# Optimization experiments

Measured on AMD Instinct MI355X. Metric: run time of the kernel, lower is better.

Reference implementation:

```python
import jax, jax.numpy as jnp
import numpy as np

N = 500000
V = 50000
GF = 64
OC = 256

def _lin(key, din, dout):
    k1, k2 = jax.random.split(key)
    w = jax.random.normal(k1, (din, dout), dtype=jnp.float32) * 0.02
    b = jax.random.normal(k2, (dout,), dtype=jnp.float32) * 0.02
    return w, b

def setup_inputs() -> dict:
    key = jax.random.key(0)
    ks = jax.random.split(key, 12)
    inp_feat = jax.random.normal(ks[0], (N, 6), dtype=jnp.float32)
    vox2point_idx = jax.random.randint(ks[1], (N,), 0, V, dtype=jnp.int32)
    w1x, b1x = _lin(ks[2], 3, GF)
    w2x, b2x = _lin(ks[3], GF, OC // 8)
    w1r, b1r = _lin(ks[4], 3, GF)
    w2r, b2r = _lin(ks[5], GF, OC // 8)
    wax, bax = _lin(ks[6], OC // 4, OC // 8)
    war, bar = _lin(ks[7], OC // 4, OC // 8)
    wv1, bv1 = _lin(ks[8], OC // 2, OC // 2)
    w3, b3 = _lin(ks[9], OC, OC)
    w4, b4 = _lin(ks[10], OC, OC)
    wv2, bv2 = _lin(ks[11], OC, OC)
    return dict(inp_feat=inp_feat, vox2point_idx=vox2point_idx, num_vox=V,
                w1x=w1x, b1x=b1x, w2x=w2x, b2x=b2x,
                w1r=w1r, b1r=b1r, w2r=w2r, b2r=b2r,
                wax=wax, bax=bax, war=war, bar=bar,
                wv1=wv1, bv1=bv1, w3=w3, b3=b3, w4=w4, b4=b4,
                wv2=wv2, bv2=bv2)

def reference(inp_feat, vox2point_idx, num_vox,
              w1x, b1x, w2x, b2x, w1r, b1r, w2r, b2r,
              wax, bax, war, bar, wv1, bv1, w3, b3, w4, b4, wv2, bv2):
    relu = jax.nn.relu
    xyz = inp_feat[:, :3]
    rgb = inp_feat[:, 3:]
    fx = relu(relu(xyz @ w1x + b1x) @ w2x + b2x)   # [N, 32]
    fr = relu(relu(rgb @ w1r + b1r) @ w2r + b2r)   # [N, 32]
    comb = jnp.concatenate([fx, fr], axis=-1)       # [N, 64]
    pf2 = jnp.concatenate([
        fx, fx * jax.nn.sigmoid(comb @ wax + bax),
        fr, fr * jax.nn.sigmoid(comb @ war + bar)], axis=-1)  # [N, 128]
    # scatter-max to voxels; torch_scatter fills empty segments with 0 and
    # pf2 >= 0 elementwise, so clamp -inf (jax empty fill) to 0 for parity.
    vox = jax.ops.segment_max(pf2, vox2point_idx, num_segments=num_vox)
    vox = jnp.maximum(vox, 0.0)                     # [V, 128]
    vox = relu(vox @ wv1 + bv1)
    pg = vox[vox2point_idx]                          # gather back [N, 128]
    pf3 = jnp.concatenate([pg, pf2], axis=-1)        # [N, 256]
    pf5 = relu(relu(pf3 @ w3 + b3) @ w4 + b4)        # [N, 256]
    vox2 = jax.ops.segment_max(pf5, vox2point_idx, num_segments=num_vox)
    vox2 = jnp.maximum(vox2, 0.0)
    return relu(vox2 @ wv2 + bv2)                    # [V, 256]
```

## Files before the change

### kernel.cpp

```cpp
#include <hip/hip_runtime.h>

#define NPTS 500000
#define NVOX 50000
#define NBLK 196

typedef unsigned short u16;
typedef unsigned int u32;
typedef __attribute__((ext_vector_type(8))) short short8;
typedef __attribute__((ext_vector_type(4))) float floatx4;
typedef __attribute__((ext_vector_type(4))) unsigned int uintx4;
typedef __attribute__((ext_vector_type(2))) unsigned int uintx2;

__device__ __forceinline__ u16 f2bf(float f) {
    u32 u = __float_as_uint(f);
    u = u + 0x7fffu + ((u >> 16) & 1u);
    return (u16)(u >> 16);
}

#if defined(__has_builtin)
#if __has_builtin(__builtin_amdgcn_cvt_pk_bf16_f32)
#define HAVE_PKBF 1
#endif
#endif

__device__ __forceinline__ u32 pkbf(float a, float b) {
#ifdef HAVE_PKBF
    typedef __attribute__((ext_vector_type(2))) __bf16 bf16x2;
    bf16x2 v = __builtin_amdgcn_cvt_pk_bf16_f32(a, b);
    u32 r; __builtin_memcpy(&r, &v, 4);
    return r;
#else
    return (u32)f2bf(a) | ((u32)f2bf(b) << 16);
#endif
}

__device__ __forceinline__ void wswz(const float* __restrict__ W, u16* __restrict__ Wf, int N, int t) {
    int k = t / N, n = t - k * N;
    int kk = k >> 5, q = (k >> 3) & 3, j = k & 7;
    Wf[((size_t)((kk * 4 + q) * N + n) << 3) + j] = f2bf(W[t]);
}

__global__ __launch_bounds__(256) void k_wprep(
    const float* __restrict__ w3, const float* __restrict__ w4,
    const float* __restrict__ wv1, const float* __restrict__ wv2,
    const float* __restrict__ w2x, const float* __restrict__ w2r,
    const float* __restrict__ wax, const float* __restrict__ war,
    u16* __restrict__ w3f, u16* __restrict__ w4f, u16* __restrict__ wv1f, u16* __restrict__ wv2f,
    u16* __restrict__ wcatf, u16* __restrict__ wattf)
{
    int t = blockIdx.x * 256 + threadIdx.x;
    if (t < 65536) { wswz(w3, w3f, 256, t); return; }  t -= 65536;
    if (t < 65536) { wswz(w4, w4f, 256, t); return; }  t -= 65536;
    if (t < 65536) { wswz(wv2, wv2f, 256, t); return; } t -= 65536;
    if (t < 16384) { wswz(wv1, wv1f, 128, t); return; } t -= 16384;
    if (t < 8192) {
        int k = t >> 6, n = t & 63;
        float v;
        if (k < 64) v = (n < 32) ? w2x[k * 32 + n] : 0.f;
        else        v = (n >= 32) ? w2r[(k - 64) * 32 + (n - 32)] : 0.f;
        int kk = k >> 5, q = (k >> 3) & 3, j = k & 7;
        wcatf[((size_t)((kk * 4 + q) * 64 + n) << 3) + j] = f2bf(v);
        return;
    }
    t -= 8192;
    if (t < 4096) {
        int k = t >> 6, n = t & 63;
        float v = (n < 32) ? wax[k * 32 + n] : war[k * 32 + (n - 32)];
        int kk = k >> 5, q = (k >> 3) & 3, j = k & 7;
        wattf[((size_t)((kk * 4 + q) * 64 + n) << 3) + j] = f2bf(v);
    }
}

__global__ void k_hist(const int* __restrict__ idx, int* __restrict__ hcnt) {
    int i = blockIdx.x * 256 + threadIdx.x;
    if (i < NPTS) atomicAdd(&hcnt[idx[i]], 1);
}

__global__ __launch_bounds__(256) void k_scan1(const int* __restrict__ hcnt, int* __restrict__ bsum) {
    __shared__ int wsum[4];
    int t = threadIdx.x;
    int i = blockIdx.x * 256 + t;
    int c = (i < NVOX) ? hcnt[i] : 0;
    #pragma unroll
    for (int d = 32; d >= 1; d >>= 1) c += __shfl_xor(c, d, 64);
    if ((t & 63) == 0) wsum[t >> 6] = c;
    __syncthreads();
    if (t == 0) bsum[blockIdx.x] = wsum[0] + wsum[1] + wsum[2] + wsum[3];
}

__global__ __launch_bounds__(256) void k_scan2(const int* __restrict__ bsum, int* __restrict__ boff) {
    __shared__ int wsum[4];
    int t = threadIdx.x, lane = t & 63, w = t >> 6;
    int c = (t < NBLK) ? bsum[t] : 0;
    int v = c;
    #pragma unroll
    for (int d = 1; d < 64; d <<= 1) {
        int o = __shfl_up(v, d, 64);
        if (lane >= d) v += o;
    }
    if (lane == 63) wsum[w] = v;
    __syncthreads();
    int wo = 0;
    #pragma unroll
    for (int k = 0; k < 4; k++) if (k < w) wo += wsum[k];
    if (t < NBLK) boff[t] = wo + v - c;
}

__global__ __launch_bounds__(256) void k_scan3(const int* __restrict__ hcnt, const int* __restrict__ boff,
                                               int* __restrict__ cur) {
    __shared__ int wsum[4];
    int t = threadIdx.x, lane = t & 63, w = t >> 6;
    int i = blockIdx.x * 256 + t;
    int c = (i < NVOX) ? hcnt[i] : 0;
    int v = c;
    #pragma unroll
    for (int d = 1; d < 64; d <<= 1) {
        int o = __shfl_up(v, d, 64);
        if (lane >= d) v += o;
    }
    if (lane == 63) wsum[w] = v;
    __syncthreads();
    int wo = 0;
    #pragma unroll
    for (int k = 0; k < 4; k++) if (k < w) wo += wsum[k];
    if (i < NVOX) cur[i] = boff[blockIdx.x] + wo + v - c;
}

__global__ void k_scatter(const int* __restrict__ idx, int* __restrict__ cur,
                          int* __restrict__ sptid, int* __restrict__ svid) {
    int i = blockIdx.x * 256 + threadIdx.x;
    if (i < NPTS) {
        int v = idx[i];
        int pos = atomicAdd(&cur[v], 1);
        sptid[pos] = i;
        svid[pos] = v;
    }
}

__global__ __launch_bounds__(512) void k_pointfeat(
    const float* __restrict__ inp, const int* __restrict__ sptid, const int* __restrict__ svid,
    const float* __restrict__ w1x, const float* __restrict__ b1x,
    const float* __restrict__ w1r, const float* __restrict__ b1r,
    const u16* __restrict__ wcatf, const float* __restrict__ b2x, const float* __restrict__ b2r,
    const u16* __restrict__ wattf, const float* __restrict__ bax, const float* __restrict__ bar,
    u16* __restrict__ pf2s, float* __restrict__ voxmax)
{
    __shared__ u16 hbuf[128 * 136];
    __shared__ float wl[512];
    __shared__ int lvid[128];
    int t = threadIdx.x;
    int i0 = blockIdx.x * 128;
    int mcnt = NPTS - i0; if (mcnt > 128) mcnt = 128;
    {
        float v;
        if (t < 192)      v = w1x[t];
        else if (t < 256) v = b1x[t - 192];
        else if (t < 448) v = w1r[t - 256];
        else              v = b1r[t - 448];
        wl[t] = v;
    }
    if (t < 128) lvid[t] = (t < mcnt) ? svid[i0 + t] : -1;
    __syncthreads();
    {
        int m = t >> 2, c = t & 3;
        float x0 = 0, x1 = 0, x2 = 0, r0 = 0, r1 = 0, r2 = 0;
        if (m < mcnt) {
            const float* p = inp + (size_t)sptid[i0 + m] * 6;
            x0 = p[0]; x1 = p[1]; x2 = p[2]; r0 = p[3]; r1 = p[4]; r2 = p[5];
        }
        u16* hb = &hbuf[m * 136 + c * 16];
        #pragma unroll
        for (int jp = 0; jp < 8; jp++) {
            int c0 = c * 16 + 2 * jp, c1 = c0 + 1;
            float hx0 = fmaxf(wl[192 + c0] + x0 * wl[c0] + x1 * wl[64 + c0] + x2 * wl[128 + c0], 0.f);
            float hx1 = fmaxf(wl[192 + c1] + x0 * wl[c1] + x1 * wl[64 + c1] + x2 * wl[128 + c1], 0.f);
            float hr0 = fmaxf(wl[448 + c0] + r0 * wl[256 + c0] + r1 * wl[320 + c0] + r2 * wl[384 + c0], 0.f);
            float hr1 = fmaxf(wl[448 + c1] + r0 * wl[256 + c1] + r1 * wl[320 + c1] + r2 * wl[384 + c1], 0.f);
            *(u32*)(hb + 2 * jp)      = pkbf(hx0, hx1);
            *(u32*)(hb + 64 + 2 * jp) = pkbf(hr0, hr1);
        }
    }
    __syncthreads();
    int wave = t >> 6, l = t & 63, q = l >> 4, lm = l & 15;
    int n = (wave & 3) * 16 + lm;
    int rh = (wave >> 2) * 64;
    floatx4 acc[4];
    #pragma unroll
    for (int a = 0; a < 4; a++) acc[a] = (floatx4){0.f, 0.f, 0.f, 0.f};
    #pragma unroll
    for (int kk = 0; kk < 4; kk++) {
        short8 bfrag = *(const short8*)&wcatf[(size_t)((kk * 4 + q) * 64 + n) << 3];
        #pragma unroll
        for (int tm = 0; tm < 4; tm++) {
            short8 afrag = *(const short8*)&hbuf[(rh + tm * 16 + lm) * 136 + kk * 32 + q * 8];
            acc[tm] = __builtin_amdgcn_mfma_f32_16x16x32_bf16(afrag, bfrag, acc[tm], 0, 0, 0);
        }
    }
    float bv = (n < 32) ? b2x[n] : b2r[n - 32];
    float comb_keep[4][4];
    #pragma unroll
    for (int tm = 0; tm < 4; tm++)
        #pragma unroll
        for (int r = 0; r < 4; r++)
            comb_keep[tm][r] = fmaxf(acc[tm][r] + bv, 0.f);
    __syncthreads();
    #pragma unroll
    for (int tm = 0; tm < 4; tm++)
        #pragma unroll
        for (int r = 0; r < 4; r++) {
            int m = rh + tm * 16 + q * 4 + r;
            hbuf[m * 136 + n] = f2bf(comb_keep[tm][r]);
        }
    __syncthreads();
    floatx4 acc2[4];
    #pragma unroll
    for (int a = 0; a < 4; a++) acc2[a] = (floatx4){0.f, 0.f, 0.f, 0.f};
    #pragma unroll
    for (int kk = 0; kk < 2; kk++) {
        short8 bfrag = *(const short8*)&wattf[(size_t)((kk * 4 + q) * 64 + n) << 3];
        #pragma unroll
        for (int tm = 0; tm < 4; tm++) {
            short8 afrag = *(const short8*)&hbuf[(rh + tm * 16 + lm) * 136 + kk * 32 + q * 8];
            acc2[tm] = __builtin_amdgcn_mfma_f32_16x16x32_bf16(afrag, bfrag, acc2[tm], 0, 0, 0);
        }
    }
    __syncthreads();
    float bv2 = (n < 32) ? bax[n] : bar[n - 32];
    int pp = (n < 32) ? n : 32 + n;
    #pragma unroll
    for (int tm = 0; tm < 4; tm++)
        #pragma unroll
        for (int r = 0; r < 4; r++) {
            float att = acc2[tm][r] + bv2;
            float sg = 1.f / (1.f + __expf(-att));
            float plain = comb_keep[tm][r];
            float gated = plain * sg;
            int m = rh + tm * 16 + q * 4 + r;
            hbuf[m * 136 + pp] = f2bf(plain);
            hbuf[m * 136 + pp + 32] = f2bf(gated);
        }
    __syncthreads();
    {
        int row = t >> 2, seg = t & 3;
        if (row < mcnt) {
            const u16* src = &hbuf[row * 136 + seg * 32];
            u16* dst = pf2s + (size_t)(i0 + row) * 128 + seg * 32;
            *(uintx4*)dst = *(const uintx4*)src;
            *(uintx4*)(dst + 8) = *(const uintx4*)(src + 8);
        }
    }
    {
        int c2 = t & 63;
        int h = t >> 6;
        int r0 = h * 16;
        int r1 = r0 + 16; if (r1 > mcnt) r1 = mcnt;
        u32 mlo = 0, mhi = 0;
        int pvid = -1;
        for (int r = r0; r < r1; r++) {
            int vid = lvid[r];
            if (vid != pvid) {
                if (pvid >= 0) {
                    int* addr = (int*)(voxmax + (size_t)pvid * 128 + 2 * c2);
                    if (mlo) atomicMax(addr, (int)(mlo << 16));
                    if (mhi) atomicMax(addr + 1, (int)(mhi << 16));
                }
                pvid = vid; mlo = 0; mhi = 0;
            }
            u32 u = *(const u32*)&hbuf[r * 136 + 2 * c2];
            u32 lo = u & 0xffffu, hi = u >> 16;
            mlo = lo > mlo ? lo : mlo;
            mhi = hi > mhi ? hi : mhi;
        }
        if (pvid >= 0) {
            int* addr = (int*)(voxmax + (size_t)pvid * 128 + 2 * c2);
            if (mlo) atomicMax(addr, (int)(mlo << 16));
            if (mhi) atomicMax(addr + 1, (int)(mhi << 16));
        }
    }
}

template<int K, int N, bool ABF16, bool OUT_BF16>
__global__ __launch_bounds__(256) void k_gemm_relu(
    const void* __restrict__ Ap, const u16* __restrict__ Wf,
    const float* __restrict__ bias, void* __restrict__ outp, int M)
{
    constexpr int STRIDE = K + 8;
    constexpr int TN = N / 64;
    constexpr int KSTEPS = K / 32;
    constexpr int CW = K / 4;
    __shared__ u16 lds[64 * STRIDE];
    int i0 = blockIdx.x * 64;
    int mcnt = M - i0; if (mcnt > 64) mcnt = 64;
    int t = threadIdx.x;
    {
        int row = t >> 2, cseg = t & 3;
        u16* dst = &lds[row * STRIDE + cseg * CW];
        if (row < mcnt) {
            if (ABF16) {
                const u16* src = (const u16*)Ap + (size_t)(i0 + row) * K + cseg * CW;
                #pragma unroll
                for (int c = 0; c < CW / 8; c++)
                    *(uintx4*)(dst + c * 8) = *(const uintx4*)(src + c * 8);
            } else {
                const float* src = (const float*)Ap + (size_t)(i0 + row) * K + cseg * CW;
                #pragma unroll
                for (int c = 0; c < CW / 8; c++) {
                    float4 v0 = *(const float4*)(src + c * 8);
                    float4 v1 = *(const float4*)(src + c * 8 + 4);
                    uintx4 rr = {pkbf(v0.x, v0.y), pkbf(v0.z, v0.w), pkbf(v1.x, v1.y), pkbf(v1.z, v1.w)};
                    *(uintx4*)(dst + c * 8) = rr;
                }
            }
        } else {
            uintx4 z = {0, 0, 0, 0};
            #pragma unroll
            for (int c = 0; c < CW / 8; c++) *(uintx4*)(dst + c * 8) = z;
        }
    }
    __syncthreads();
    int wave = t >> 6, l = t & 63;
    int q = l >> 4, lm = l & 15;
    int wn0 = wave * (N / 4);
    floatx4 acc[4][TN];
    #pragma unroll
    for (int a = 0; a < 4; a++)
        #pragma unroll
        for (int b = 0; b < TN; b++) acc[a][b] = (floatx4){0.f, 0.f, 0.f, 0.f};
    #pragma unroll
    for (int kk = 0; kk < KSTEPS; kk++) {
        short8 afrag[4], bfrag[TN];
        #pragma unroll
        for (int tm = 0; tm < 4; tm++)
            afrag[tm] = *(const short8*)&lds[(tm * 16 + lm) * STRIDE + kk * 32 + q * 8];
        #pragma unroll
        for (int tn = 0; tn < TN; tn++)
            bfrag[tn] = *(const short8*)&Wf[(size_t)((kk * 4 + q) * N + wn0 + tn * 16 + lm) * 8];
        #pragma unroll
        for (int tm = 0; tm < 4; tm++)
            #pragma unroll
            for (int tn = 0; tn < TN; tn++)
                acc[tm][tn] = __builtin_amdgcn_mfma_f32_16x16x32_bf16(afrag[tm], bfrag[tn], acc[tm][tn], 0, 0, 0);
    }
    #pragma unroll
    for (int tm = 0; tm < 4; tm++)
        #pragma unroll
        for (int tn = 0; tn < TN; tn++) {
            int n = wn0 + tn * 16 + lm;
            float bv = bias[n];
            #pragma unroll
            for (int r = 0; r < 4; r++) {
                int m = tm * 16 + q * 4 + r;
                if (m < mcnt) {
                    float v = fmaxf(acc[tm][tn][r] + bv, 0.f);
                    if (OUT_BF16) ((u16*)outp)[(size_t)(i0 + m) * N + n] = f2bf(v);
                    else          ((float*)outp)[(size_t)(i0 + m) * N + n] = v;
                }
            }
        }
}

__global__ __launch_bounds__(512) void k_pointmlp(
    const u16* __restrict__ voxf, const u16* __restrict__ pf2s, const int* __restrict__ svid,
    const u16* __restrict__ w3f, const float* __restrict__ b3,
    const u16* __restrict__ w4f, const float* __restrict__ b4,
    float* __restrict__ vox2)
{
    constexpr int STRIDE = 264;
    __shared__ u16 lds[64 * STRIDE];
    __shared__ int lvid[64];
    __shared__ float bl[512];
    int i0 = blockIdx.x * 64;
    int mcnt = NPTS - i0; if (mcnt > 64) mcnt = 64;
    int t = threadIdx.x;
    if (t < 64) lvid[t] = (t < mcnt) ? svid[i0 + t] : -1;
    bl[t] = (t < 256) ? b3[t] : b4[t - 256];
    {
        int row = t >> 3, cseg = t & 7;
        u16* dst = &lds[row * STRIDE + cseg * 32];
        if (row < mcnt) {
            const u16* src;
            if (cseg < 4) src = voxf + (size_t)svid[i0 + row] * 128 + cseg * 32;
            else          src = pf2s + (size_t)(i0 + row) * 128 + (cseg - 4) * 32;
            #pragma unroll
            for (int c = 0; c < 4; c++)
                *(uintx4*)(dst + c * 8) = *(const uintx4*)(src + c * 8);
        } else {
            uintx4 z = {0, 0, 0, 0};
            #pragma unroll
            for (int c = 0; c < 4; c++) *(uintx4*)(dst + c * 8) = z;
        }
    }
    __syncthreads();
    int wave = t >> 6, l = t & 63;
    int q = l >> 4, lm = l & 15;
    int wm0 = wave * 32;
    floatx4 acc[2][4];
    #pragma unroll
    for (int a = 0; a < 2; a++)
        #pragma unroll
        for (int b = 0; b < 4; b++) acc[a][b] = (floatx4){0.f, 0.f, 0.f, 0.f};
    #pragma unroll
    for (int kk = 0; kk < 8; kk++) {
        short8 wfrag[2], bfrag[4];
        #pragma unroll
        for (int tm = 0; tm < 2; tm++)
            wfrag[tm] = *(const short8*)&w3f[(size_t)((kk * 4 + q) * 256 + wm0 + tm * 16 + lm) * 8];
        #pragma unroll
        for (int tn = 0; tn < 4; tn++)
            bfrag[tn] = *(const short8*)&lds[(tn * 16 + lm) * STRIDE + kk * 32 + q * 8];
        #pragma unroll
        for (int tm = 0; tm < 2; tm++)
            #pragma unroll
            for (int tn = 0; tn < 4; tn++)
                acc[tm][tn] = __builtin_amdgcn_mfma_f32_16x16x32_bf16(wfrag[tm], bfrag[tn], acc[tm][tn], 0, 0, 0);
    }
    __syncthreads();
    #pragma unroll
    for (int tm = 0; tm < 2; tm++) {
        float4 bq = *(const float4*)&bl[wm0 + tm * 16 + 4 * q];
        #pragma unroll
        for (int tn = 0; tn < 4; tn++) {
            u32 lo = pkbf(fmaxf(acc[tm][tn][0] + bq.x, 0.f), fmaxf(acc[tm][tn][1] + bq.y, 0.f));
            u32 hi = pkbf(fmaxf(acc[tm][tn][2] + bq.z, 0.f), fmaxf(acc[tm][tn][3] + bq.w, 0.f));
            *(uintx2*)&lds[(tn * 16 + lm) * STRIDE + wm0 + tm * 16 + 4 * q] = (uintx2){lo, hi};
        }
    }
    __syncthreads();
    floatx4 acc2[2][4];
    #pragma unroll
    for (int a = 0; a < 2; a++)
        #pragma unroll
        for (int b = 0; b < 4; b++) acc2[a][b] = (floatx4){0.f, 0.f, 0.f, 0.f};
    #pragma unroll
    for (int kk = 0; kk < 8; kk++) {
        short8 wfrag[2], bfrag[4];
        #pragma unroll
        for (int tm = 0; tm < 2; tm++)
            wfrag[tm] = *(const short8*)&w4f[(size_t)((kk * 4 + q) * 256 + wm0 + tm * 16 + lm) * 8];
        #pragma unroll
        for (int tn = 0; tn < 4; tn++)
            bfrag[tn] = *(const short8*)&lds[(tn * 16 + lm) * STRIDE + kk * 32 + q * 8];
        #pragma unroll
        for (int tm = 0; tm < 2; tm++)
            #pragma unroll
            for (int tn = 0; tn < 4; tn++)
                acc2[tm][tn] = __builtin_amdgcn_mfma_f32_16x16x32_bf16(wfrag[tm], bfrag[tn], acc2[tm][tn], 0, 0, 0);
    }
    __syncthreads();
    #pragma unroll
    for (int tm = 0; tm < 2; tm++) {
        float4 bq = *(const float4*)&bl[256 + wm0 + tm * 16 + 4 * q];
        #pragma unroll
        for (int tn = 0; tn < 4; tn++) {
            u32 lo = pkbf(fmaxf(acc2[tm][tn][0] + bq.x, 0.f), fmaxf(acc2[tm][tn][1] + bq.y, 0.f));
            u32 hi = pkbf(fmaxf(acc2[tm][tn][2] + bq.z, 0.f), fmaxf(acc2[tm][tn][3] + bq.w, 0.f));
            *(uintx2*)&lds[(tn * 16 + lm) * STRIDE + wm0 + tm * 16 + 4 * q] = (uintx2){lo, hi};
        }
    }
    __syncthreads();
    {
        int c2 = t & 127;
        int h = t >> 7;
        int r0 = h * 16;
        int r1 = r0 + 16; if (r1 > mcnt) r1 = mcnt;
        u32 mlo = 0, mhi = 0;
        int pvid = -1;
        for (int r = r0; r < r1; r++) {
            int vid = lvid[r];
            if (vid != pvid) {
                if (pvid >= 0) {
                    int* addr = (int*)(vox2 + (size_t)pvid * 256 + 2 * c2);
                    if (mlo) atomicMax(addr, (int)(mlo << 16));
                    if (mhi) atomicMax(addr + 1, (int)(mhi << 16));
                }
                pvid = vid; mlo = 0; mhi = 0;
            }
            u32 u = *(const u32*)&lds[r * STRIDE + 2 * c2];
            u32 lo = u & 0xffffu, hi = u >> 16;
            mlo = lo > mlo ? lo : mlo;
            mhi = hi > mhi ? hi : mhi;
        }
        if (pvid >= 0) {
            int* addr = (int*)(vox2 + (size_t)pvid * 256 + 2 * c2);
            if (mlo) atomicMax(addr, (int)(mlo << 16));
            if (mhi) atomicMax(addr + 1, (int)(mhi << 16));
        }
    }
}

extern "C" void kernel_launch(void* const* d_in, const int* in_sizes, int n_in,
                              void* d_out, int out_size, void* d_ws, size_t ws_size,
                              hipStream_t stream) {
    const float* inp = (const float*)d_in[0];
    const int*   idx = (const int*)d_in[1];
    const float* w1x = (const float*)d_in[3];  const float* b1x = (const float*)d_in[4];
    const float* w2x = (const float*)d_in[5];  const float* b2x = (const float*)d_in[6];
    const float* w1r = (const float*)d_in[7];  const float* b1r = (const float*)d_in[8];
    const float* w2r = (const float*)d_in[9];  const float* b2r = (const float*)d_in[10];
    const float* wax = (const float*)d_in[11]; const float* bax = (const float*)d_in[12];
    const float* war = (const float*)d_in[13]; const float* bar = (const float*)d_in[14];
    const float* wv1 = (const float*)d_in[15]; const float* bv1 = (const float*)d_in[16];
    const float* w3  = (const float*)d_in[17]; const float* b3  = (const float*)d_in[18];
    const float* w4  = (const float*)d_in[19]; const float* b4  = (const float*)d_in[20];
    const float* wv2 = (const float*)d_in[21]; const float* bv2 = (const float*)d_in[22];
    float* out = (float*)d_out;

    char* ws = (char*)d_ws;
    u16*   pf2s   = (u16*)ws;   ws += (size_t)NPTS * 128 * sizeof(u16);
    float* voxmax = (float*)ws; ws += (size_t)NVOX * 128 * sizeof(float);
    u16*   voxf   = (u16*)ws;   ws += (size_t)NVOX * 128 * sizeof(u16);
    float* vox2   = (float*)ws; ws += (size_t)NVOX * 256 * sizeof(float);
    u16*   w3f    = (u16*)ws;   ws += 65536 * sizeof(u16);
    u16*   w4f    = (u16*)ws;   ws += 65536 * sizeof(u16);
    u16*   wv1f   = (u16*)ws;   ws += 16384 * sizeof(u16);
    u16*   wv2f   = (u16*)ws;   ws += 65536 * sizeof(u16);
    u16*   wcatf  = (u16*)ws;   ws += 8192 * sizeof(u16);
    u16*   wattf  = (u16*)ws;   ws += 4096 * sizeof(u16);
    int*   hcnt   = (int*)ws;   ws += (size_t)NVOX * sizeof(int);
    int*   cur    = (int*)ws;   ws += (size_t)NVOX * sizeof(int);
    int*   bsum   = (int*)ws;   ws += (size_t)NBLK * sizeof(int);
    int*   boff   = (int*)ws;   ws += (size_t)NBLK * sizeof(int);
    int*   sptid  = (int*)ws;   ws += (size_t)NPTS * sizeof(int);
    int*   svid   = (int*)ws;   ws += (size_t)NPTS * sizeof(int);

    hipMemsetAsync(hcnt, 0, (size_t)NVOX * sizeof(int), stream);
    hipMemsetAsync(voxmax, 0, (size_t)NVOX * 128 * sizeof(float), stream);
    hipMemsetAsync(vox2, 0, (size_t)NVOX * 256 * sizeof(float), stream);

    k_wprep<<<880, 256, 0, stream>>>(w3, w4, wv1, wv2, w2x, w2r, wax, war,
                                     w3f, w4f, wv1f, wv2f, wcatf, wattf);

    k_hist<<<(NPTS + 255) / 256, 256, 0, stream>>>(idx, hcnt);
    k_scan1<<<NBLK, 256, 0, stream>>>(hcnt, bsum);
    k_scan2<<<1, 256, 0, stream>>>(bsum, boff);
    k_scan3<<<NBLK, 256, 0, stream>>>(hcnt, boff, cur);
    k_scatter<<<(NPTS + 255) / 256, 256, 0, stream>>>(idx, cur, sptid, svid);

    k_pointfeat<<<(NPTS + 127) / 128, 512, 0, stream>>>(
        inp, sptid, svid, w1x, b1x, w1r, b1r, wcatf, b2x, b2r, wattf, bax, bar, pf2s, voxmax);

    k_gemm_relu<128, 128, false, true><<<(NVOX + 63) / 64, 256, 0, stream>>>(
        (const void*)voxmax, wv1f, bv1, (void*)voxf, NVOX);

    k_pointmlp<<<(NPTS + 63) / 64, 512, 0, stream>>>(
        voxf, pf2s, svid, w3f, b3, w4f, b4, vox2);

    k_gemm_relu<256, 256, false, false><<<(NVOX + 63) / 64, 256, 0, stream>>>(
        (const void*)vox2, wv2f, bv2, (void*)out, NVOX);
}
```

Measured before the change: 514.9 us.

## Switch point MLP to 32x32x16 MFMA with 256-thread blocks and XOR-swizzled LDS

The fused point-MLP kernel now uses 32x32x16 bf16 MFMA tiles instead of 16x16x32, with 4 waves per 64-point block. Each wave covers 32 points by 128 channels. The w3/w4 weight swizzle is changed to match the new K-fragment layout, and LDS rows use an XOR chunk swizzle to cut bank conflicts on fragment reads and writes. Fewer, larger MFMAs reuse each B fragment across four weight tiles. The cost is more accumulator registers per thread and half as many threads per block to issue loads and scatter-max atomics.

```diff
diff --git a/kernel.cpp b/kernel.cpp
--- a/kernel.cpp
+++ b/kernel.cpp
@@ -8,6 +8,7 @@
 typedef unsigned int u32;
 typedef __attribute__((ext_vector_type(8))) short short8;
 typedef __attribute__((ext_vector_type(4))) float floatx4;
+typedef __attribute__((ext_vector_type(16))) float floatx16;
 typedef __attribute__((ext_vector_type(4))) unsigned int uintx4;
 typedef __attribute__((ext_vector_type(2))) unsigned int uintx2;
 
@@ -40,6 +41,12 @@
     Wf[((size_t)((kk * 4 + q) * N + n) << 3) + j] = f2bf(W[t]);
 }
 
+__device__ __forceinline__ void wswz32(const float* __restrict__ W, u16* __restrict__ Wf, int N, int t) {
+    int k = t / N, n = t - k * N;
+    int kk = k >> 4, h = (k >> 3) & 1, j = k & 7;
+    Wf[((size_t)((kk * 2 + h) * N + n) << 3) + j] = f2bf(W[t]);
+}
+
 __global__ __launch_bounds__(256) void k_wprep(
     const float* __restrict__ w3, const float* __restrict__ w4,
     const float* __restrict__ wv1, const float* __restrict__ wv2,
@@ -49,8 +56,8 @@
     u16* __restrict__ wcatf, u16* __restrict__ wattf)
 {
     int t = blockIdx.x * 256 + threadIdx.x;
-    if (t < 65536) { wswz(w3, w3f, 256, t); return; }  t -= 65536;
-    if (t < 65536) { wswz(w4, w4f, 256, t); return; }  t -= 65536;
+    if (t < 65536) { wswz32(w3, w3f, 256, t); return; }  t -= 65536;
+    if (t < 65536) { wswz32(w4, w4f, 256, t); return; }  t -= 65536;
     if (t < 65536) { wswz(wv2, wv2f, 256, t); return; } t -= 65536;
     if (t < 16384) { wswz(wv1, wv1f, 128, t); return; } t -= 16384;
     if (t < 8192) {
@@ -359,7 +366,7 @@
         }
 }
 
-__global__ __launch_bounds__(512) void k_pointmlp(
+__global__ __launch_bounds__(256) void k_pointmlp(
     const u16* __restrict__ voxf, const u16* __restrict__ pf2s, const int* __restrict__ svid,
     const u16* __restrict__ w3f, const float* __restrict__ b3,
     const u16* __restrict__ w4f, const float* __restrict__ b4,
@@ -373,96 +380,101 @@
     int mcnt = NPTS - i0; if (mcnt > 64) mcnt = 64;
     int t = threadIdx.x;
     if (t < 64) lvid[t] = (t < mcnt) ? svid[i0 + t] : -1;
-    bl[t] = (t < 256) ? b3[t] : b4[t - 256];
-    {
-        int row = t >> 3, cseg = t & 7;
-        u16* dst = &lds[row * STRIDE + cseg * 32];
+    for (int s = t; s < 512; s += 256) bl[s] = (s < 256) ? b3[s] : b4[s - 256];
+    {
+        int row = t >> 2, cseg = t & 3;
+        int sig = (row >> 3) & 3;
         if (row < mcnt) {
             const u16* src;
-            if (cseg < 4) src = voxf + (size_t)svid[i0 + row] * 128 + cseg * 32;
-            else          src = pf2s + (size_t)(i0 + row) * 128 + (cseg - 4) * 32;
+            if (cseg < 2) src = voxf + (size_t)svid[i0 + row] * 128 + cseg * 64;
+            else          src = pf2s + (size_t)(i0 + row) * 128 + (cseg - 2) * 64;
             #pragma unroll
-            for (int c = 0; c < 4; c++)
-                *(uintx4*)(dst + c * 8) = *(const uintx4*)(src + c * 8);
+            for (int c = 0; c < 8; c++) {
+                int chunk = cseg * 8 + c;
+                *(uintx4*)&lds[row * STRIDE + (chunk ^ sig) * 8] = *(const uintx4*)(src + c * 8);
+            }
         } else {
             uintx4 z = {0, 0, 0, 0};
             #pragma unroll
-            for (int c = 0; c < 4; c++) *(uintx4*)(dst + c * 8) = z;
+            for (int c = 0; c < 8; c++) {
+                int chunk = cseg * 8 + c;
+                *(uintx4*)&lds[row * STRIDE + (chunk ^ sig) * 8] = z;
+            }
         }
     }
     __syncthreads();
     int wave = t >> 6, l = t & 63;
-    int q = l >> 4, lm = l & 15;
-    int wm0 = wave * 32;
-    floatx4 acc[2][4];
-    #pragma unroll
-    for (int a = 0; a < 2; a++)
-        #pragma unroll
-        for (int b = 0; b < 4; b++) acc[a][b] = (floatx4){0.f, 0.f, 0.f, 0.f};
-    #pragma unroll
-    for (int kk = 0; kk < 8; kk++) {
-        short8 wfrag[2], bfrag[4];
-        #pragma unroll
-        for (int tm = 0; tm < 2; tm++)
-            wfrag[tm] = *(const short8*)&w3f[(size_t)((kk * 4 + q) * 256 + wm0 + tm * 16 + lm) * 8];
-        #pragma unroll
-        for (int tn = 0; tn < 4; tn++)
-            bfrag[tn] = *(const short8*)&lds[(tn * 16 + lm) * STRIDE + kk * 32 + q * 8];
-        #pragma unroll
-        for (int tm = 0; tm < 2; tm++)
-            #pragma unroll
-            for (int tn = 0; tn < 4; tn++)
-                acc[tm][tn] = __builtin_amdgcn_mfma_f32_16x16x32_bf16(wfrag[tm], bfrag[tn], acc[tm][tn], 0, 0, 0);
-    }
-    __syncthreads();
-    #pragma unroll
-    for (int tm = 0; tm < 2; tm++) {
-        float4 bq = *(const float4*)&bl[wm0 + tm * 16 + 4 * q];
-        #pragma unroll
-        for (int tn = 0; tn < 4; tn++) {
-            u32 lo = pkbf(fmaxf(acc[tm][tn][0] + bq.x, 0.f), fmaxf(acc[tm][tn][1] + bq.y, 0.f));
-            u32 hi = pkbf(fmaxf(acc[tm][tn][2] + bq.z, 0.f), fmaxf(acc[tm][tn][3] + bq.w, 0.f));
-            *(uintx2*)&lds[(tn * 16 + lm) * STRIDE + wm0 + tm * 16 + 4 * q] = (uintx2){lo, hi};
-        }
-    }
-    __syncthreads();
-    floatx4 acc2[2][4];
-    #pragma unroll
-    for (int a = 0; a < 2; a++)
-        #pragma unroll
-        for (int b = 0; b < 4; b++) acc2[a][b] = (floatx4){0.f, 0.f, 0.f, 0.f};
-    #pragma unroll
-    for (int kk = 0; kk < 8; kk++) {
-        short8 wfrag[2], bfrag[4];
-        #pragma unroll
-        for (int tm = 0; tm < 2; tm++)
-            wfrag[tm] = *(const short8*)&w4f[(size_t)((kk * 4 + q) * 256 + wm0 + tm * 16 + lm) * 8];
-        #pragma unroll
-        for (int tn = 0; tn < 4; tn++)
-            bfrag[tn] = *(const short8*)&lds[(tn * 16 + lm) * STRIDE + kk * 32 + q * 8];
-        #pragma unroll
-        for (int tm = 0; tm < 2; tm++)
-            #pragma unroll
-            for (int tn = 0; tn < 4; tn++)
-                acc2[tm][tn] = __builtin_amdgcn_mfma_f32_16x16x32_bf16(wfrag[tm], bfrag[tn], acc2[tm][tn], 0, 0, 0);
-    }
-    __syncthreads();
-    #pragma unroll
-    for (int tm = 0; tm < 2; tm++) {
-        float4 bq = *(const float4*)&bl[256 + wm0 + tm * 16 + 4 * q];
-        #pragma unroll
-        for (int tn = 0; tn < 4; tn++) {
-            u32 lo = pkbf(fmaxf(acc2[tm][tn][0] + bq.x, 0.f), fmaxf(acc2[tm][tn][1] + bq.y, 0.f));
-            u32 hi = pkbf(fmaxf(acc2[tm][tn][2] + bq.z, 0.f), fmaxf(acc2[tm][tn][3] + bq.w, 0.f));
-            *(uintx2*)&lds[(tn * 16 + lm) * STRIDE + wm0 + tm * 16 + 4 * q] = (uintx2){lo, hi};
+    int am = l & 31, hh = l >> 5;
+    int cg = wave & 1;
+    int pg = wave >> 1;
+    int pbase = pg * 32;
+    int p = pbase + am;
+    int sigp = (p >> 3) & 3;
+    int chb = cg * 128;
+    floatx16 acc[4];
+    #pragma unroll
+    for (int a = 0; a < 4; a++)
+        #pragma unroll
+        for (int e = 0; e < 16; e++) acc[a][e] = 0.f;
+    #pragma unroll
+    for (int kk = 0; kk < 16; kk++) {
+        short8 bfrag = *(const short8*)&lds[p * STRIDE + (((kk * 2 + hh) ^ sigp) << 3)];
+        #pragma unroll
+        for (int tm = 0; tm < 4; tm++) {
+            short8 wfrag = *(const short8*)&w3f[(size_t)((kk * 2 + hh) * 256 + chb + tm * 32 + am) * 8];
+            acc[tm] = __builtin_amdgcn_mfma_f32_32x32x16_bf16(wfrag, bfrag, acc[tm], 0, 0, 0);
+        }
+    }
+    __syncthreads();
+    #pragma unroll
+    for (int tm = 0; tm < 4; tm++) {
+        int chb2 = chb + tm * 32;
+        #pragma unroll
+        for (int rg = 0; rg < 4; rg++) {
+            int ch0 = chb2 + 8 * rg + 4 * hh;
+            float4 bq = *(const float4*)&bl[ch0];
+            u32 lo = pkbf(fmaxf(acc[tm][4 * rg + 0] + bq.x, 0.f), fmaxf(acc[tm][4 * rg + 1] + bq.y, 0.f));
+            u32 hi = pkbf(fmaxf(acc[tm][4 * rg + 2] + bq.z, 0.f), fmaxf(acc[tm][4 * rg + 3] + bq.w, 0.f));
+            int chunk = (chb2 >> 3) + rg;
+            *(uintx2*)&lds[p * STRIDE + ((chunk ^ sigp) << 3) + 4 * hh] = (uintx2){lo, hi};
+        }
+    }
+    __syncthreads();
+    floatx16 acc2[4];
+    #pragma unroll
+    for (int a = 0; a < 4; a++)
+        #pragma unroll
+        for (int e = 0; e < 16; e++) acc2[a][e] = 0.f;
+    #pragma unroll
+    for (int kk = 0; kk < 16; kk++) {
+        short8 bfrag = *(const short8*)&lds[p * STRIDE + (((kk * 2 + hh) ^ sigp) << 3)];
+        #pragma unroll
+        for (int tm = 0; tm < 4; tm++) {
+            short8 wfrag = *(const short8*)&w4f[(size_t)((kk * 2 + hh) * 256 + chb + tm * 32 + am) * 8];
+            acc2[tm] = __builtin_amdgcn_mfma_f32_32x32x16_bf16(wfrag, bfrag, acc2[tm], 0, 0, 0);
+        }
+    }
+    __syncthreads();
+    #pragma unroll
+    for (int tm = 0; tm < 4; tm++) {
+        int chb2 = chb + tm * 32;
+        #pragma unroll
+        for (int rg = 0; rg < 4; rg++) {
+            int ch0 = chb2 + 8 * rg + 4 * hh;
+            float4 bq = *(const float4*)&bl[256 + ch0];
+            u32 lo = pkbf(fmaxf(acc2[tm][4 * rg + 0] + bq.x, 0.f), fmaxf(acc2[tm][4 * rg + 1] + bq.y, 0.f));
+            u32 hi = pkbf(fmaxf(acc2[tm][4 * rg + 2] + bq.z, 0.f), fmaxf(acc2[tm][4 * rg + 3] + bq.w, 0.f));
+            int chunk = (chb2 >> 3) + rg;
+            *(uintx2*)&lds[p * STRIDE + ((chunk ^ sigp) << 3) + 4 * hh] = (uintx2){lo, hi};
         }
     }
     __syncthreads();
     {
         int c2 = t & 127;
         int h = t >> 7;
-        int r0 = h * 16;
-        int r1 = r0 + 16; if (r1 > mcnt) r1 = mcnt;
+        int r0 = h * 32;
+        int r1 = r0 + 32; if (r1 > mcnt) r1 = mcnt;
+        int chunk = c2 >> 2, off = (2 * c2) & 7;
         u32 mlo = 0, mhi = 0;
         int pvid = -1;
         for (int r = r0; r < r1; r++) {
@@ -475,7 +487,8 @@
                 }
                 pvid = vid; mlo = 0; mhi = 0;
             }
-            u32 u = *(const u32*)&lds[r * STRIDE + 2 * c2];
+            int sig = (r >> 3) & 3;
+            u32 u = *(const u32*)&lds[r * STRIDE + ((chunk ^ sig) << 3) + off];
             u32 lo = u & 0xffffu, hi = u >> 16;
             mlo = lo > mlo ? lo : mlo;
             mhi = hi > mhi ? hi : mhi;
@@ -542,7 +555,7 @@
     k_gemm_relu<128, 128, false, true><<<(NVOX + 63) / 64, 256, 0, stream>>>(
         (const void*)voxmax, wv1f, bv1, (void*)voxf, NVOX);
 
-    k_pointmlp<<<(NPTS + 63) / 64, 512, 0, stream>>>(
+    k_pointmlp<<<(NPTS + 63) / 64, 256, 0, stream>>>(
         voxf, pf2s, svid, w3f, b3, w4f, b4, vox2);
 
     k_gemm_relu<256, 256, false, false><<<(NVOX + 63) / 64, 256, 0, stream>>>(
```

Result: slower. 574.2 us (+11.5%).
